# Optimization experiments

Hardware: AMD Instinct MI355X
Metric: run time of the kernel (lower is better)

## Reference

```python
import jax, jax.numpy as jnp
from jax import lax
import numpy as np

TAPS = 4          # db2 filter length
LEVEL = 4
CH = 32
SLOPE = 10.0      # sigmoid sharpness of learned hard-threshold activation

# db2 decomposition low-pass coefficients (pywt convention)
_DB2 = np.array([-0.12940952255126037, 0.2241438680420134,
                 0.8365163037378079, 0.48296291314453416], dtype=np.float32)

def setup_inputs() -> dict:
    key = jax.random.key(0)
    k1, k2, k3 = jax.random.split(key, 3)
    x = jax.random.normal(k1, (128, CH, 4096), dtype=jnp.float32)
    # learned per-channel, per-level low-pass kernels: db2 init + small perturbation
    h_lo = jnp.asarray(_DB2)[None, None, :] + 0.02 * jax.random.normal(
        k2, (CH, LEVEL, TAPS), dtype=jnp.float32)
    # learned symmetric thresholds (Act_Init=0 -> small positive values)
    bias = 0.1 * jax.random.uniform(k3, (CH, LEVEL), dtype=jnp.float32)
    return {"x": x, "h_lo": h_lo, "bias": bias}

def _grouped_dwt_step(a, k_lo, k_hi):
    # a: [B,C,T]; kernels: [C,1,taps]; circular boundary, stride-2 downsample
    B, C, T = a.shape
    a_pad = jnp.concatenate([a, a[..., : TAPS - 1]], axis=-1)  # circular pad
    dn = ('NCH', 'OIH', 'NCH')
    lo = lax.conv_general_dilated(a_pad, k_lo, (2,), 'VALID',
                                  dimension_numbers=dn, feature_group_count=C)
    hi = lax.conv_general_dilated(a_pad, k_hi, (2,), 'VALID',
                                  dimension_numbers=dn, feature_group_count=C)
    return lo, hi  # each [B,C,T//2]

def reference(x, h_lo, bias):
    """Batched learned wavelet decomposition (all channels at once via grouped conv).
    Returns coefficients packed along last dim: [yl, d_L, ..., d_1] -> [B,C,T].
    """
    B, C, T = x.shape
    sign = ((-1.0) ** jnp.arange(TAPS)).astype(x.dtype)  # QMF sign flip
    a = x
    details = []
    for l in range(LEVEL):
        k_lo = h_lo[:, l, :][:, None, :]                       # [C,1,taps]
        k_hi = (sign * h_lo[:, l, ::-1])[:, None, :]           # high-pass via QMF
        a, hi = _grouped_dwt_step(a, k_lo, k_hi)
        b = bias[None, :, l, None]                             # [1,C,1]
        # symmetric sigmoid (soft hard-threshold) activation on detail coeffs
        d = hi * (jax.nn.sigmoid(SLOPE * (hi - b)) + jax.nn.sigmoid(-SLOPE * (hi + b)))
        details.append(d)
    # pack: approximation (coarsest) first, then details coarsest->finest
    return jnp.concatenate([a] + details[::-1], axis=-1)
```

## Files before the change

kernel.cpp:

```cpp
#include <hip/hip_runtime.h>
#include <math.h>

#define TLEN 4096
#define LEVELS 4
#define CHANS 32
#define SLOPE 10.0f

__device__ __forceinline__ float sgate(float hi, float b) {
    const float za = fminf(fmaxf(-SLOPE * (hi - b), -30.f), 30.f);
    const float zb = fminf(fmaxf( SLOPE * (hi + b), -30.f), 30.f);
    const float ea = __expf(za);
    const float eb = __expf(zb);
    return hi * (2.f + ea + eb) * __builtin_amdgcn_rcpf((1.f + ea) * (1.f + eb));
}

__global__ __launch_bounds__(256) void lwpt_kernel(
    const float* __restrict__ x, const float* __restrict__ h_lo,
    const float* __restrict__ bias, float* __restrict__ out)
{
    __shared__ float bufA[2048];
    __shared__ float bufB[1024];

    const int bc  = blockIdx.x;
    const int c   = bc & (CHANS - 1);
    const int tid = threadIdx.x;

    const float* xrow = x   + (size_t)bc * TLEN;
    float*       orow = out + (size_t)bc * TLEN;

    const float4 k0v = ((const float4*)h_lo)[c * LEVELS + 0];
    const float4 k1v = ((const float4*)h_lo)[c * LEVELS + 1];
    const float4 k2v = ((const float4*)h_lo)[c * LEVELS + 2];
    const float4 k3v = ((const float4*)h_lo)[c * LEVELS + 3];
    const float b0 = bias[c * LEVELS + 0];
    const float b1 = bias[c * LEVELS + 1];
    const float b2 = bias[c * LEVELS + 2];
    const float b3 = bias[c * LEVELS + 3];

    {
        const float4* x4 = (const float4*)xrow;
        float in[18];
        #pragma unroll
        for (int k = 0; k < 4; ++k) {
            const float4 v = x4[4 * tid + k];
            in[4*k+0] = v.x; in[4*k+1] = v.y; in[4*k+2] = v.z; in[4*k+3] = v.w;
        }
        const float2 e = *(const float2*)(xrow + ((16 * tid + 16) & (TLEN - 1)));
        in[16] = e.x; in[17] = e.y;

        float lo[8], dd[8];
        #pragma unroll
        for (int j = 0; j < 8; ++j) {
            const float a0 = in[2*j], a1 = in[2*j+1], a2 = in[2*j+2], a3 = in[2*j+3];
            lo[j] = a0*k0v.x + a1*k0v.y + a2*k0v.z + a3*k0v.w;
            const float hi = a0*k0v.w - a1*k0v.z + a2*k0v.y - a3*k0v.x;
            dd[j] = sgate(hi, b0);
        }
        ((float4*)bufA)[2*tid]   = make_float4(lo[0], lo[1], lo[2], lo[3]);
        ((float4*)bufA)[2*tid+1] = make_float4(lo[4], lo[5], lo[6], lo[7]);
        float4* o4 = (float4*)(orow + 2048);
        o4[2*tid]   = make_float4(dd[0], dd[1], dd[2], dd[3]);
        o4[2*tid+1] = make_float4(dd[4], dd[5], dd[6], dd[7]);
    }
    __syncthreads();

    {
        float in[10];
        #pragma unroll
        for (int k = 0; k < 2; ++k) {
            const float4 v = ((const float4*)bufA)[2 * tid + k];
            in[4*k+0] = v.x; in[4*k+1] = v.y; in[4*k+2] = v.z; in[4*k+3] = v.w;
        }
        const float2 e = *(const float2*)(bufA + ((8 * tid + 8) & 2047));
        in[8] = e.x; in[9] = e.y;

        float lo[4], dd[4];
        #pragma unroll
        for (int j = 0; j < 4; ++j) {
            const float a0 = in[2*j], a1 = in[2*j+1], a2 = in[2*j+2], a3 = in[2*j+3];
            lo[j] = a0*k1v.x + a1*k1v.y + a2*k1v.z + a3*k1v.w;
            const float hi = a0*k1v.w - a1*k1v.z + a2*k1v.y - a3*k1v.x;
            dd[j] = sgate(hi, b1);
        }
        ((float4*)bufB)[tid] = make_float4(lo[0], lo[1], lo[2], lo[3]);
        ((float4*)(orow + 1024))[tid] = make_float4(dd[0], dd[1], dd[2], dd[3]);
    }
    __syncthreads();

    {
        float in[6];
        const float4 v = ((const float4*)bufB)[tid];
        in[0] = v.x; in[1] = v.y; in[2] = v.z; in[3] = v.w;
        const float2 e = *(const float2*)(bufB + ((4 * tid + 4) & 1023));
        in[4] = e.x; in[5] = e.y;

        float lo[2], dd[2];
        #pragma unroll
        for (int j = 0; j < 2; ++j) {
            const float a0 = in[2*j], a1 = in[2*j+1], a2 = in[2*j+2], a3 = in[2*j+3];
            lo[j] = a0*k2v.x + a1*k2v.y + a2*k2v.z + a3*k2v.w;
            const float hi = a0*k2v.w - a1*k2v.z + a2*k2v.y - a3*k2v.x;
            dd[j] = sgate(hi, b2);
        }
        ((float2*)bufA)[tid] = make_float2(lo[0], lo[1]);
        ((float2*)(orow + 512))[tid] = make_float2(dd[0], dd[1]);
    }
    __syncthreads();

    {
        const float a0 = bufA[2 * tid];
        const float a1 = bufA[2 * tid + 1];
        const float2 e = *(const float2*)(bufA + ((2 * tid + 2) & 511));
        const float a2 = e.x, a3 = e.y;
        const float lo = a0*k3v.x + a1*k3v.y + a2*k3v.z + a3*k3v.w;
        const float hi = a0*k3v.w - a1*k3v.z + a2*k3v.y - a3*k3v.x;
        orow[tid]       = lo;
        orow[256 + tid] = sgate(hi, b3);
    }
}

extern "C" void kernel_launch(void* const* d_in, const int* in_sizes, int n_in,
                              void* d_out, int out_size, void* d_ws, size_t ws_size,
                              hipStream_t stream) {
    const float* x    = (const float*)d_in[0];
    const float* h_lo = (const float*)d_in[1];
    const float* bias = (const float*)d_in[2];
    float* out = (float*)d_out;

    dim3 grid(128 * CHANS);
    dim3 block(256);
    lwpt_kernel<<<grid, block, 0, stream>>>(x, h_lo, bias, out);
}
```

Measured before the change: 26.08 us.

## Fuse last two DWT levels into one wavefront with shuffles and nontemporal stores

Levels 3 and 4 are now computed by a single 64-lane wavefront. Each lane handles 8 level-3 outputs and gets its level-4 neighbours through a cross-lane shuffle, which removes one shared-memory round trip and one block barrier. All output stores become nontemporal 128-bit stores, and the clamp uses fmed3. The cost is that only a quarter of the threads are busy during the tail levels.

```diff
diff --git a/kernel.cpp b/kernel.cpp
--- a/kernel.cpp
+++ b/kernel.cpp
@@ -6,12 +6,21 @@
 #define CHANS 32
 #define SLOPE 10.0f
 
+typedef float vfloat4 __attribute__((ext_vector_type(4)));
+
+__device__ __forceinline__ float clamp30(float v) {
+    return __builtin_amdgcn_fmed3f(v, -30.f, 30.f);
+}
+
 __device__ __forceinline__ float sgate(float hi, float b) {
-    const float za = fminf(fmaxf(-SLOPE * (hi - b), -30.f), 30.f);
-    const float zb = fminf(fmaxf( SLOPE * (hi + b), -30.f), 30.f);
-    const float ea = __expf(za);
-    const float eb = __expf(zb);
+    const float ea = __expf(clamp30(-SLOPE * (hi - b)));
+    const float eb = __expf(clamp30( SLOPE * (hi + b)));
     return hi * (2.f + ea + eb) * __builtin_amdgcn_rcpf((1.f + ea) * (1.f + eb));
+}
+
+__device__ __forceinline__ void nt_store4(float* p, float a, float b, float c, float d) {
+    vfloat4 v = { a, b, c, d };
+    __builtin_nontemporal_store(v, (vfloat4*)p);
 }
 
 __global__ __launch_bounds__(256) void lwpt_kernel(
@@ -30,12 +39,8 @@
 
     const float4 k0v = ((const float4*)h_lo)[c * LEVELS + 0];
     const float4 k1v = ((const float4*)h_lo)[c * LEVELS + 1];
-    const float4 k2v = ((const float4*)h_lo)[c * LEVELS + 2];
-    const float4 k3v = ((const float4*)h_lo)[c * LEVELS + 3];
     const float b0 = bias[c * LEVELS + 0];
     const float b1 = bias[c * LEVELS + 1];
-    const float b2 = bias[c * LEVELS + 2];
-    const float b3 = bias[c * LEVELS + 3];
 
     {
         const float4* x4 = (const float4*)xrow;
@@ -58,9 +63,8 @@
         }
         ((float4*)bufA)[2*tid]   = make_float4(lo[0], lo[1], lo[2], lo[3]);
         ((float4*)bufA)[2*tid+1] = make_float4(lo[4], lo[5], lo[6], lo[7]);
-        float4* o4 = (float4*)(orow + 2048);
-        o4[2*tid]   = make_float4(dd[0], dd[1], dd[2], dd[3]);
-        o4[2*tid+1] = make_float4(dd[4], dd[5], dd[6], dd[7]);
+        nt_store4(orow + 2048 + 8*tid,     dd[0], dd[1], dd[2], dd[3]);
+        nt_store4(orow + 2048 + 8*tid + 4, dd[4], dd[5], dd[6], dd[7]);
     }
     __syncthreads();
 
@@ -83,39 +87,53 @@
             dd[j] = sgate(hi, b1);
         }
         ((float4*)bufB)[tid] = make_float4(lo[0], lo[1], lo[2], lo[3]);
-        ((float4*)(orow + 1024))[tid] = make_float4(dd[0], dd[1], dd[2], dd[3]);
+        nt_store4(orow + 1024 + 4*tid, dd[0], dd[1], dd[2], dd[3]);
     }
     __syncthreads();
 
-    {
-        float in[6];
-        const float4 v = ((const float4*)bufB)[tid];
-        in[0] = v.x; in[1] = v.y; in[2] = v.z; in[3] = v.w;
-        const float2 e = *(const float2*)(bufB + ((4 * tid + 4) & 1023));
-        in[4] = e.x; in[5] = e.y;
+    if (tid < 64) {
+        const int lane = tid;
+        const float4 k2v = ((const float4*)h_lo)[c * LEVELS + 2];
+        const float4 k3v = ((const float4*)h_lo)[c * LEVELS + 3];
+        const float b2 = bias[c * LEVELS + 2];
+        const float b3 = bias[c * LEVELS + 3];
 
-        float lo[2], dd[2];
+        float in[18];
         #pragma unroll
-        for (int j = 0; j < 2; ++j) {
+        for (int k = 0; k < 4; ++k) {
+            const float4 v = ((const float4*)bufB)[4 * lane + k];
+            in[4*k+0] = v.x; in[4*k+1] = v.y; in[4*k+2] = v.z; in[4*k+3] = v.w;
+        }
+        const float2 e = *(const float2*)(bufB + ((16 * lane + 16) & 1023));
+        in[16] = e.x; in[17] = e.y;
+
+        float lo3[8], dd3[8];
+        #pragma unroll
+        for (int j = 0; j < 8; ++j) {
             const float a0 = in[2*j], a1 = in[2*j+1], a2 = in[2*j+2], a3 = in[2*j+3];
-            lo[j] = a0*k2v.x + a1*k2v.y + a2*k2v.z + a3*k2v.w;
+            lo3[j] = a0*k2v.x + a1*k2v.y + a2*k2v.z + a3*k2v.w;
             const float hi = a0*k2v.w - a1*k2v.z + a2*k2v.y - a3*k2v.x;
-            dd[j] = sgate(hi, b2);
+            dd3[j] = sgate(hi, b2);
         }
-        ((float2*)bufA)[tid] = make_float2(lo[0], lo[1]);
-        ((float2*)(orow + 512))[tid] = make_float2(dd[0], dd[1]);
-    }
-    __syncthreads();
+        nt_store4(orow + 512 + 8*lane,     dd3[0], dd3[1], dd3[2], dd3[3]);
+        nt_store4(orow + 512 + 8*lane + 4, dd3[4], dd3[5], dd3[6], dd3[7]);
 
-    {
-        const float a0 = bufA[2 * tid];
-        const float a1 = bufA[2 * tid + 1];
-        const float2 e = *(const float2*)(bufA + ((2 * tid + 2) & 511));
-        const float a2 = e.x, a3 = e.y;
-        const float lo = a0*k3v.x + a1*k3v.y + a2*k3v.z + a3*k3v.w;
-        const float hi = a0*k3v.w - a1*k3v.z + a2*k3v.y - a3*k3v.x;
-        orow[tid]       = lo;
-        orow[256 + tid] = sgate(hi, b3);
+        const int nxt = (lane + 1) & 63;
+        const float n0 = __shfl(lo3[0], nxt, 64);
+        const float n1 = __shfl(lo3[1], nxt, 64);
+        float lo4[4], dd4[4];
+        #pragma unroll
+        for (int j = 0; j < 4; ++j) {
+            const float a0 = lo3[2*j];
+            const float a1 = lo3[2*j+1];
+            const float a2 = (2*j+2 < 8) ? lo3[2*j+2] : n0;
+            const float a3 = (2*j+3 < 8) ? lo3[2*j+3] : n1;
+            lo4[j] = a0*k3v.x + a1*k3v.y + a2*k3v.z + a3*k3v.w;
+            const float hi = a0*k3v.w - a1*k3v.z + a2*k3v.y - a3*k3v.x;
+            dd4[j] = sgate(hi, b3);
+        }
+        nt_store4(orow + 4*lane,       lo4[0], lo4[1], lo4[2], lo4[3]);
+        nt_store4(orow + 256 + 4*lane, dd4[0], dd4[1], dd4[2], dd4[3]);
     }
 }
 
```

Measured after the change: 28.81 us. +10.5%, slower.
